# Kernel tuning notes

Measured on AMD Instinct MI355X. Metric: run time of the kernel, lower is better.

Reference implementation:

```python
import jax, jax.numpy as jnp
import numpy as np

E, K, H, F = 16, 4, 1024, 2048
SL, BS = 2048, 2
ALPHA, LIMIT = 1.702, 7.0
CAPACITY_FACTOR = 1.0


def setup_inputs() -> dict:
    key = jax.random.key(0)
    ks = jax.random.split(key, 7)
    x = jax.random.normal(ks[0], (SL, BS, H), jnp.float32)
    router_weight = jax.random.normal(ks[1], (E, H), jnp.float32) * 0.02
    router_bias = jax.random.normal(ks[2], (E,), jnp.float32) * 0.02
    w1 = jax.random.normal(ks[3], (E, H, 2 * F), jnp.float32) * 0.02
    w2 = jax.random.normal(ks[4], (E, F, H), jnp.float32) * 0.02
    w1_bias = jax.random.normal(ks[5], (E, 2 * F), jnp.float32) * 0.02
    w2_bias = jax.random.normal(ks[6], (E, H), jnp.float32) * 0.02
    return {"x": x, "router_weight": router_weight, "router_bias": router_bias,
            "w1": w1, "w2": w2, "w1_bias": w1_bias, "w2_bias": w2_bias}


def reference(x, router_weight, router_bias, w1, w2, w1_bias, w2_bias):
    sl, bs, h = x.shape
    T = sl * bs                      # total tokens
    N = T * K                        # total routed copies
    C = int(CAPACITY_FACTOR * K * T / E)  # static expert capacity
    xf = x.reshape(T, h)

    # --- route_tokens ---
    logits = xf @ router_weight.T + router_bias            # [T, E]
    expert_weights, expert_indices = jax.lax.top_k(logits, K)  # [T, K]
    expert_weights = jax.nn.softmax(expert_weights, axis=-1)
    router_scores = jnp.zeros_like(logits).at[
        jnp.arange(T)[:, None], expert_indices].set(expert_weights).T  # [E, T]

    # --- indices_and_bins: stable sort by expert + histogram ---
    te = expert_indices.reshape(-1)                        # [N] expert id per copy
    ew = expert_weights.reshape(-1)                        # [N] weight per copy
    order = jnp.argsort(te)                                # stable sort -> permutation
    tokens_per_expert = jnp.zeros((E,), jnp.int32).at[te].add(1)
    starts = jnp.cumsum(tokens_per_expert) - tokens_per_expert  # exclusive cumsum

    # --- binned_gather: [E, C, H], overflow tokens dropped, underfull slots zero ---
    j = jnp.arange(C)
    pos = starts[:, None] + j[None, :]                     # [E, C] position in sorted order
    valid = j[None, :] < tokens_per_expert[:, None]        # [E, C]
    flat_idx = order[jnp.clip(pos, 0, N - 1)]              # [E, C] index into flattened copies
    tok = flat_idx // K                                    # [E, C] source token row
    xb = jnp.where(valid[..., None], xf[tok], 0.0)         # [E, C, H]

    # --- mlp_forward: interleaved GLU ---
    gate_up = jnp.einsum('ech,ehf->ecf', xb, w1) + w1_bias[:, None, :]  # [E, C, 2F]
    gate = jnp.minimum(gate_up[..., ::2], LIMIT)
    up = jnp.clip(gate_up[..., 1::2], -LIMIT, LIMIT)
    glu = gate * jax.nn.sigmoid(gate * ALPHA)
    y = jnp.einsum('ecf,efh->ech', (up + 1.0) * glu, w2) + w2_bias[:, None, :]  # [E, C, H]

    # --- binned_scatter: weighted combine back to token rows ---
    w = jnp.where(valid, ew[flat_idx], 0.0)                # [E, C]
    out = jnp.zeros((T, h), x.dtype).at[tok.reshape(-1)].add(
        (w[..., None] * y).reshape(-1, h))
    return out.reshape(sl, bs, h), expert_weights, router_scores
```

## Files before the change

kernel.cpp:

```cpp
#include <hip/hip_runtime.h>
#include <hip/hip_bf16.h>

#define T_TOK 4096
#define E_EXP 16
#define TOPK 4
#define HDIM 1024
#define FDIM 2048
#define CAP 1024
#define NCOPY (T_TOK*TOPK)

typedef __bf16 bf16x8 __attribute__((ext_vector_type(8)));
typedef __bf16 bf16x4 __attribute__((ext_vector_type(4)));
typedef float  f32x4  __attribute__((ext_vector_type(4)));

__global__ __launch_bounds__(64) void router_kernel(
    const float* __restrict__ x, const float* __restrict__ rw, const float* __restrict__ rb,
    float* __restrict__ ew_out, float* __restrict__ rs_out, int* __restrict__ te_out)
{
    int t = blockIdx.x;
    int lane = threadIdx.x;
    const float* xr = x + (size_t)t * HDIM;
    float xv[16];
#pragma unroll
    for (int i = 0; i < 16; ++i) xv[i] = xr[i * 64 + lane];
    float lg[E_EXP];
#pragma unroll
    for (int e = 0; e < E_EXP; ++e) {
        const float* wrow = rw + (size_t)e * HDIM;
        float s = 0.f;
#pragma unroll
        for (int i = 0; i < 16; ++i) s += xv[i] * wrow[i * 64 + lane];
#pragma unroll
        for (int off = 32; off > 0; off >>= 1) s += __shfl_xor(s, off, 64);
        lg[e] = s + rb[e];
    }
    int mask = 0; float vals[4]; int idxs[4];
#pragma unroll
    for (int k = 0; k < 4; ++k) {
        float m = -3.4e38f; int a = 0;
#pragma unroll
        for (int e = 0; e < E_EXP; ++e) {
            bool take = (((mask >> e) & 1) == 0) && (lg[e] > m);
            m = take ? lg[e] : m;
            a = take ? e : a;
        }
        vals[k] = m; idxs[k] = a; mask |= (1 << a);
    }
    float wk[4]; float ssum = 0.f;
#pragma unroll
    for (int k = 0; k < 4; ++k) { wk[k] = __expf(vals[k] - vals[0]); ssum += wk[k]; }
    float inv = 1.f / ssum;
#pragma unroll
    for (int k = 0; k < 4; ++k) wk[k] *= inv;
    if (lane < 4) {
        float wv = 0.f; int iv = 0;
#pragma unroll
        for (int k = 0; k < 4; ++k) if (lane == k) { wv = wk[k]; iv = idxs[k]; }
        ew_out[t * 4 + lane] = wv;
        te_out[t * 4 + lane] = iv;
    }
    if (lane < E_EXP) {
        float v = 0.f;
#pragma unroll
        for (int k = 0; k < 4; ++k) v = (idxs[k] == lane) ? wk[k] : v;
        rs_out[(size_t)lane * T_TOK + t] = v;
    }
}

__global__ __launch_bounds__(256) void binning_kernel(
    const int* __restrict__ te, const float* __restrict__ ew,
    int* __restrict__ slot_tok, float* __restrict__ slot_w)
{
    __shared__ int cnt[256][17];
    int tid = threadIdx.x;
#pragma unroll
    for (int e = 0; e < E_EXP; ++e) cnt[tid][e] = 0;
    __syncthreads();
    int base = tid * 64;
    for (int i = 0; i < 64; ++i) cnt[tid][te[base + i]]++;
    __syncthreads();
    if (tid < E_EXP) {
        int run = 0;
        for (int t2 = 0; t2 < 256; ++t2) { int v = cnt[t2][tid]; cnt[t2][tid] = run; run += v; }
    }
    __syncthreads();
    for (int s = tid; s < E_EXP * CAP; s += 256) { slot_tok[s] = -1; slot_w[s] = 0.f; }
    __syncthreads();
    for (int i = 0; i < 64; ++i) {
        int idx = base + i;
        int e = te[idx];
        int r = cnt[tid][e]; cnt[tid][e] = r + 1;
        if (r < CAP) { slot_tok[e * CAP + r] = idx >> 2; slot_w[e * CAP + r] = ew[idx]; }
    }
}

__global__ __launch_bounds__(256) void gather_kernel(
    const float* __restrict__ x, const int* __restrict__ slot_tok, __bf16* __restrict__ xg)
{
    int s = blockIdx.x, tid = threadIdx.x;
    int tok = slot_tok[s];
    bf16x4 o;
    if (tok >= 0) {
        float4 v = *(const float4*)(x + (size_t)tok * HDIM + tid * 4);
        o[0] = (__bf16)v.x; o[1] = (__bf16)v.y; o[2] = (__bf16)v.z; o[3] = (__bf16)v.w;
    } else {
        o[0] = (__bf16)0.f; o[1] = (__bf16)0.f; o[2] = (__bf16)0.f; o[3] = (__bf16)0.f;
    }
    *(bf16x4*)(xg + (size_t)s * HDIM + tid * 4) = o;
}

__global__ __launch_bounds__(256) void transpose_cvt_kernel(
    const float* __restrict__ in, __bf16* __restrict__ out, int R, int Cc, int tilesR, int tilesC)
{
    __shared__ __bf16 tile[64][68];
    int bx = blockIdx.x;
    int tpe = tilesR * tilesC;
    int e = bx / tpe; int rem = bx - e * tpe;
    int tr = rem / tilesC; int tc = rem - tr * tilesC;
    const float* ine = in + (size_t)e * R * Cc;
    __bf16* oute = out + (size_t)e * R * Cc;
    int r0 = tr * 64, c0 = tc * 64;
    int tid = threadIdx.x;
    int rr = tid >> 4, c4 = (tid & 15) << 2;
#pragma unroll
    for (int it = 0; it < 4; ++it) {
        int r = rr + it * 16;
        float4 v = *(const float4*)(ine + (size_t)(r0 + r) * Cc + c0 + c4);
        tile[r][c4 + 0] = (__bf16)v.x; tile[r][c4 + 1] = (__bf16)v.y;
        tile[r][c4 + 2] = (__bf16)v.z; tile[r][c4 + 3] = (__bf16)v.w;
    }
    __syncthreads();
#pragma unroll
    for (int it = 0; it < 4; ++it) {
        int c = rr + it * 16;
        bf16x4 o;
        o[0] = tile[c4 + 0][c]; o[1] = tile[c4 + 1][c];
        o[2] = tile[c4 + 2][c]; o[3] = tile[c4 + 3][c];
        *(bf16x4*)(oute + (size_t)(c0 + c) * R + r0 + c4) = o;
    }
}

__global__ __launch_bounds__(256) void zero_kernel(float4* p)
{
    p[(size_t)blockIdx.x * 256 + threadIdx.x] = make_float4(0.f, 0.f, 0.f, 0.f);
}

template <int EPI>
__global__ __launch_bounds__(256) void gemm_kernel(
    const __bf16* __restrict__ A, const __bf16* __restrict__ Bt, const float* __restrict__ bias,
    __bf16* __restrict__ actout, float* __restrict__ out,
    const int* __restrict__ slot_tok, const float* __restrict__ slot_w,
    int Kd, int tilesM, int tilesN, int N)
{
    __shared__ __bf16 at[128 * 32];
    __shared__ __bf16 bts[128 * 32];
    int bx = blockIdx.x;
    int tpe = tilesM * tilesN;
    int e = bx / tpe; int rem = bx - e * tpe;
    int bm = rem / tilesN; int bn = rem - bm * tilesN;
    const __bf16* Ab = A + (size_t)e * 1024 * Kd + (size_t)(bm * 128) * Kd;
    const __bf16* Bb = Bt + (size_t)e * N * Kd + (size_t)(bn * 128) * Kd;
    int tid = threadIdx.x;
    int c0 = tid, c1 = tid + 256;
    int ar0 = c0 >> 2, ak0 = (c0 & 3) << 3;
    int ar1 = c1 >> 2, ak1 = (c1 & 3) << 3;

    uint4 ra0 = *(const uint4*)(Ab + (size_t)ar0 * Kd + ak0);
    uint4 ra1 = *(const uint4*)(Ab + (size_t)ar1 * Kd + ak1);
    uint4 rb0 = *(const uint4*)(Bb + (size_t)ar0 * Kd + ak0);
    uint4 rb1 = *(const uint4*)(Bb + (size_t)ar1 * Kd + ak1);

    f32x4 zero4 = {0.f, 0.f, 0.f, 0.f};
    f32x4 acc[4][4];
#pragma unroll
    for (int mi = 0; mi < 4; ++mi)
#pragma unroll
        for (int ni = 0; ni < 4; ++ni) acc[mi][ni] = zero4;

    int w = tid >> 6, l = tid & 63;
    int q = l >> 4, ln = l & 15;
    int wr = (w >> 1) << 6, wc = (w & 1) << 6;

    for (int k0 = 0; k0 < Kd; k0 += 32) {
        *(uint4*)(at + c0 * 8) = ra0;
        *(uint4*)(at + c1 * 8) = ra1;
        *(uint4*)(bts + c0 * 8) = rb0;
        *(uint4*)(bts + c1 * 8) = rb1;
        int kn = k0 + 32;
        if (kn < Kd) {
            ra0 = *(const uint4*)(Ab + (size_t)ar0 * Kd + kn + ak0);
            ra1 = *(const uint4*)(Ab + (size_t)ar1 * Kd + kn + ak1);
            rb0 = *(const uint4*)(Bb + (size_t)ar0 * Kd + kn + ak0);
            rb1 = *(const uint4*)(Bb + (size_t)ar1 * Kd + kn + ak1);
        }
        __syncthreads();
        bf16x8 af[4], bfr[4];
#pragma unroll
        for (int mi = 0; mi < 4; ++mi)
            af[mi] = *(const bf16x8*)(at + (wr + mi * 16 + ln) * 32 + q * 8);
#pragma unroll
        for (int ni = 0; ni < 4; ++ni)
            bfr[ni] = *(const bf16x8*)(bts + (wc + ni * 16 + ln) * 32 + q * 8);
#pragma unroll
        for (int mi = 0; mi < 4; ++mi)
#pragma unroll
            for (int ni = 0; ni < 4; ++ni)
                acc[mi][ni] = __builtin_amdgcn_mfma_f32_16x16x32_bf16(af[mi], bfr[ni], acc[mi][ni], 0, 0, 0);
        __syncthreads();
    }

    float bv[4];
#pragma unroll
    for (int ni = 0; ni < 4; ++ni) bv[ni] = bias[(size_t)e * N + bn * 128 + wc + ni * 16 + ln];

    if constexpr (EPI == 0) {
        __bf16* act_e = actout + (size_t)e * 1024 * FDIM;
#pragma unroll
        for (int mi = 0; mi < 4; ++mi)
#pragma unroll
            for (int ni = 0; ni < 4; ++ni)
#pragma unroll
                for (int r = 0; r < 4; ++r) {
                    int m = bm * 128 + wr + mi * 16 + q * 4 + r;
                    int n = bn * 128 + wc + ni * 16 + ln;
                    float v = acc[mi][ni][r] + bv[ni];
                    float o = __shfl_xor(v, 1, 64);
                    float gate = (ln & 1) ? o : v;
                    float up   = (ln & 1) ? v : o;
                    gate = fminf(gate, 7.f);
                    up = fminf(fmaxf(up, -7.f), 7.f);
                    float glu = gate / (1.f + __expf(-1.702f * gate));
                    float a = (up + 1.f) * glu;
                    if ((ln & 1) == 0) act_e[(size_t)m * FDIM + (n >> 1)] = (__bf16)a;
                }
    } else {
#pragma unroll
        for (int mi = 0; mi < 4; ++mi)
#pragma unroll
            for (int r = 0; r < 4; ++r) {
                int m = bm * 128 + wr + mi * 16 + q * 4 + r;
                int tok = slot_tok[e * CAP + m];
                float wgt = slot_w[e * CAP + m];
                if (tok >= 0) {
#pragma unroll
                    for (int ni = 0; ni < 4; ++ni) {
                        int n = bn * 128 + wc + ni * 16 + ln;
                        float v = (acc[mi][ni][r] + bv[ni]) * wgt;
                        unsafeAtomicAdd(out + (size_t)tok * HDIM + n, v);
                    }
                }
            }
    }
}

extern "C" void kernel_launch(void* const* d_in, const int* in_sizes, int n_in,
                              void* d_out, int out_size, void* d_ws, size_t ws_size,
                              hipStream_t stream)
{
    const float* x  = (const float*)d_in[0];
    const float* rw = (const float*)d_in[1];
    const float* rb = (const float*)d_in[2];
    const float* w1 = (const float*)d_in[3];
    const float* w2 = (const float*)d_in[4];
    const float* b1 = (const float*)d_in[5];
    const float* b2 = (const float*)d_in[6];
    float* out_main = (float*)d_out;
    float* ew_out = out_main + (size_t)T_TOK * HDIM;
    float* rs_out = ew_out + (size_t)T_TOK * TOPK;

    char* ws = (char*)d_ws;
    size_t off = 0;
    auto alloc = [&](size_t bytes) { void* p = ws + off; off += (bytes + 255) & ~(size_t)255; return p; };
    __bf16* w1t = (__bf16*)alloc((size_t)E_EXP * 2 * FDIM * HDIM * 2);
    __bf16* w2t = (__bf16*)alloc((size_t)E_EXP * HDIM * FDIM * 2);
    __bf16* xg  = (__bf16*)alloc((size_t)E_EXP * CAP * HDIM * 2);
    __bf16* act = (__bf16*)alloc((size_t)E_EXP * CAP * FDIM * 2);
    int*   te       = (int*)alloc((size_t)NCOPY * 4);
    int*   slot_tok = (int*)alloc((size_t)E_EXP * CAP * 4);
    float* slot_w   = (float*)alloc((size_t)E_EXP * CAP * 4);

    zero_kernel<<<(T_TOK * HDIM) / 1024, 256, 0, stream>>>((float4*)out_main);
    router_kernel<<<T_TOK, 64, 0, stream>>>(x, rw, rb, ew_out, rs_out, te);
    binning_kernel<<<1, 256, 0, stream>>>(te, ew_out, slot_tok, slot_w);
    gather_kernel<<<E_EXP * CAP, 256, 0, stream>>>(x, slot_tok, xg);
    transpose_cvt_kernel<<<E_EXP * (HDIM / 64) * (2 * FDIM / 64), 256, 0, stream>>>(
        w1, w1t, HDIM, 2 * FDIM, HDIM / 64, 2 * FDIM / 64);
    transpose_cvt_kernel<<<E_EXP * (FDIM / 64) * (HDIM / 64), 256, 0, stream>>>(
        w2, w2t, FDIM, HDIM, FDIM / 64, HDIM / 64);
    gemm_kernel<0><<<E_EXP * 8 * 32, 256, 0, stream>>>(
        xg, w1t, b1, act, nullptr, nullptr, nullptr, HDIM, 8, 32, 2 * FDIM);
    gemm_kernel<1><<<E_EXP * 8 * 8, 256, 0, stream>>>(
        act, w2t, b2, nullptr, out_main, slot_tok, slot_w, FDIM, 8, 8, HDIM);
}
```

Measured before the change: 911.3 us.

## Replace atomic scatter with bf16 expert output plus gather combine; use async LDS loads

The second GEMM no longer scatters weighted results into the output with float atomics. It writes a per-expert bf16 output buffer, which reuses the gather buffer. A new combine kernel then reads each token's up to four slots, through a new slot_of map built during binning, and writes the weighted sum. This removes the output zeroing kernel and the atomic contention. The GEMM main loop now fills LDS with direct global_load_lds transfers instead of a register-staged prefetch. That drops the register staging but also removes the overlap between the next tile's load and the current tile's MFMA work. Storing the expert output in bf16 adds rounding before the combine.

```diff
diff --git a/kernel.cpp b/kernel.cpp
--- a/kernel.cpp
+++ b/kernel.cpp
@@ -13,6 +13,14 @@
 typedef __bf16 bf16x4 __attribute__((ext_vector_type(4)));
 typedef float  f32x4  __attribute__((ext_vector_type(4)));
 
+__device__ __forceinline__ void async16(const __bf16* g, __bf16* l)
+{
+    __builtin_amdgcn_global_load_lds(
+        (const __attribute__((address_space(1))) unsigned int*)g,
+        (__attribute__((address_space(3))) unsigned int*)l,
+        16, 0, 0);
+}
+
 __global__ __launch_bounds__(64) void router_kernel(
     const float* __restrict__ x, const float* __restrict__ rw, const float* __restrict__ rb,
     float* __restrict__ ew_out, float* __restrict__ rs_out, int* __restrict__ te_out)
@@ -68,8 +76,8 @@
 }
 
 __global__ __launch_bounds__(256) void binning_kernel(
-    const int* __restrict__ te, const float* __restrict__ ew,
-    int* __restrict__ slot_tok, float* __restrict__ slot_w)
+    const int* __restrict__ te,
+    int* __restrict__ slot_tok, int* __restrict__ slot_of)
 {
     __shared__ int cnt[256][17];
     int tid = threadIdx.x;
@@ -84,13 +92,14 @@
         for (int t2 = 0; t2 < 256; ++t2) { int v = cnt[t2][tid]; cnt[t2][tid] = run; run += v; }
     }
     __syncthreads();
-    for (int s = tid; s < E_EXP * CAP; s += 256) { slot_tok[s] = -1; slot_w[s] = 0.f; }
+    for (int s = tid; s < E_EXP * CAP; s += 256) slot_tok[s] = -1;
     __syncthreads();
     for (int i = 0; i < 64; ++i) {
         int idx = base + i;
         int e = te[idx];
         int r = cnt[tid][e]; cnt[tid][e] = r + 1;
-        if (r < CAP) { slot_tok[e * CAP + r] = idx >> 2; slot_w[e * CAP + r] = ew[idx]; }
+        if (r < CAP) { slot_tok[e * CAP + r] = idx >> 2; slot_of[idx] = e * CAP + r; }
+        else slot_of[idx] = -1;
     }
 }
 
@@ -140,17 +149,10 @@
     }
 }
 
-__global__ __launch_bounds__(256) void zero_kernel(float4* p)
-{
-    p[(size_t)blockIdx.x * 256 + threadIdx.x] = make_float4(0.f, 0.f, 0.f, 0.f);
-}
-
 template <int EPI>
 __global__ __launch_bounds__(256) void gemm_kernel(
     const __bf16* __restrict__ A, const __bf16* __restrict__ Bt, const float* __restrict__ bias,
-    __bf16* __restrict__ actout, float* __restrict__ out,
-    const int* __restrict__ slot_tok, const float* __restrict__ slot_w,
-    int Kd, int tilesM, int tilesN, int N)
+    __bf16* __restrict__ outp, int Kd, int tilesM, int tilesN, int N)
 {
     __shared__ __bf16 at[128 * 32];
     __shared__ __bf16 bts[128 * 32];
@@ -165,10 +167,14 @@
     int ar0 = c0 >> 2, ak0 = (c0 & 3) << 3;
     int ar1 = c1 >> 2, ak1 = (c1 & 3) << 3;
 
-    uint4 ra0 = *(const uint4*)(Ab + (size_t)ar0 * Kd + ak0);
-    uint4 ra1 = *(const uint4*)(Ab + (size_t)ar1 * Kd + ak1);
-    uint4 rb0 = *(const uint4*)(Bb + (size_t)ar0 * Kd + ak0);
-    uint4 rb1 = *(const uint4*)(Bb + (size_t)ar1 * Kd + ak1);
+    const __bf16* gA0 = Ab + (size_t)ar0 * Kd + ak0;
+    const __bf16* gA1 = Ab + (size_t)ar1 * Kd + ak1;
+    const __bf16* gB0 = Bb + (size_t)ar0 * Kd + ak0;
+    const __bf16* gB1 = Bb + (size_t)ar1 * Kd + ak1;
+    __bf16* lA0 = at + c0 * 8;
+    __bf16* lA1 = at + c1 * 8;
+    __bf16* lB0 = bts + c0 * 8;
+    __bf16* lB1 = bts + c1 * 8;
 
     f32x4 zero4 = {0.f, 0.f, 0.f, 0.f};
     f32x4 acc[4][4];
@@ -182,17 +188,10 @@
     int wr = (w >> 1) << 6, wc = (w & 1) << 6;
 
     for (int k0 = 0; k0 < Kd; k0 += 32) {
-        *(uint4*)(at + c0 * 8) = ra0;
-        *(uint4*)(at + c1 * 8) = ra1;
-        *(uint4*)(bts + c0 * 8) = rb0;
-        *(uint4*)(bts + c1 * 8) = rb1;
-        int kn = k0 + 32;
-        if (kn < Kd) {
-            ra0 = *(const uint4*)(Ab + (size_t)ar0 * Kd + kn + ak0);
-            ra1 = *(const uint4*)(Ab + (size_t)ar1 * Kd + kn + ak1);
-            rb0 = *(const uint4*)(Bb + (size_t)ar0 * Kd + kn + ak0);
-            rb1 = *(const uint4*)(Bb + (size_t)ar1 * Kd + kn + ak1);
-        }
+        async16(gA0 + k0, lA0);
+        async16(gA1 + k0, lA1);
+        async16(gB0 + k0, lB0);
+        async16(gB1 + k0, lB1);
         __syncthreads();
         bf16x8 af[4], bfr[4];
 #pragma unroll
@@ -214,7 +213,7 @@
     for (int ni = 0; ni < 4; ++ni) bv[ni] = bias[(size_t)e * N + bn * 128 + wc + ni * 16 + ln];
 
     if constexpr (EPI == 0) {
-        __bf16* act_e = actout + (size_t)e * 1024 * FDIM;
+        __bf16* act_e = outp + (size_t)e * 1024 * FDIM;
 #pragma unroll
         for (int mi = 0; mi < 4; ++mi)
 #pragma unroll
@@ -234,23 +233,38 @@
                     if ((ln & 1) == 0) act_e[(size_t)m * FDIM + (n >> 1)] = (__bf16)a;
                 }
     } else {
+        __bf16* y_e = outp + (size_t)e * 1024 * HDIM;
 #pragma unroll
         for (int mi = 0; mi < 4; ++mi)
 #pragma unroll
-            for (int r = 0; r < 4; ++r) {
-                int m = bm * 128 + wr + mi * 16 + q * 4 + r;
-                int tok = slot_tok[e * CAP + m];
-                float wgt = slot_w[e * CAP + m];
-                if (tok >= 0) {
-#pragma unroll
-                    for (int ni = 0; ni < 4; ++ni) {
-                        int n = bn * 128 + wc + ni * 16 + ln;
-                        float v = (acc[mi][ni][r] + bv[ni]) * wgt;
-                        unsafeAtomicAdd(out + (size_t)tok * HDIM + n, v);
-                    }
+            for (int ni = 0; ni < 4; ++ni)
+#pragma unroll
+                for (int r = 0; r < 4; ++r) {
+                    int m = bm * 128 + wr + mi * 16 + q * 4 + r;
+                    int n = bn * 128 + wc + ni * 16 + ln;
+                    y_e[(size_t)m * HDIM + n] = (__bf16)(acc[mi][ni][r] + bv[ni]);
                 }
-            }
-    }
+    }
+}
+
+__global__ __launch_bounds__(256) void combine_kernel(
+    const __bf16* __restrict__ y, const int* __restrict__ slot_of,
+    const float* __restrict__ ew, float* __restrict__ out)
+{
+    int t = blockIdx.x, tid = threadIdx.x;
+    float a0 = 0.f, a1 = 0.f, a2 = 0.f, a3 = 0.f;
+#pragma unroll
+    for (int k = 0; k < 4; ++k) {
+        int s = slot_of[t * 4 + k];
+        if (s >= 0) {
+            float wk = ew[t * 4 + k];
+            bf16x4 v = *(const bf16x4*)(y + (size_t)s * HDIM + tid * 4);
+            a0 += wk * (float)v[0]; a1 += wk * (float)v[1];
+            a2 += wk * (float)v[2]; a3 += wk * (float)v[3];
+        }
+    }
+    float4 o = make_float4(a0, a1, a2, a3);
+    *(float4*)(out + (size_t)t * HDIM + tid * 4) = o;
 }
 
 extern "C" void kernel_launch(void* const* d_in, const int* in_sizes, int n_in,
@@ -277,18 +291,19 @@
     __bf16* act = (__bf16*)alloc((size_t)E_EXP * CAP * FDIM * 2);
     int*   te       = (int*)alloc((size_t)NCOPY * 4);
     int*   slot_tok = (int*)alloc((size_t)E_EXP * CAP * 4);
-    float* slot_w   = (float*)alloc((size_t)E_EXP * CAP * 4);
-
-    zero_kernel<<<(T_TOK * HDIM) / 1024, 256, 0, stream>>>((float4*)out_main);
+    int*   slot_of  = (int*)alloc((size_t)NCOPY * 4);
+    __bf16* y = xg;
+
     router_kernel<<<T_TOK, 64, 0, stream>>>(x, rw, rb, ew_out, rs_out, te);
-    binning_kernel<<<1, 256, 0, stream>>>(te, ew_out, slot_tok, slot_w);
+    binning_kernel<<<1, 256, 0, stream>>>(te, slot_tok, slot_of);
     gather_kernel<<<E_EXP * CAP, 256, 0, stream>>>(x, slot_tok, xg);
     transpose_cvt_kernel<<<E_EXP * (HDIM / 64) * (2 * FDIM / 64), 256, 0, stream>>>(
         w1, w1t, HDIM, 2 * FDIM, HDIM / 64, 2 * FDIM / 64);
     transpose_cvt_kernel<<<E_EXP * (FDIM / 64) * (HDIM / 64), 256, 0, stream>>>(
         w2, w2t, FDIM, HDIM, FDIM / 64, HDIM / 64);
     gemm_kernel<0><<<E_EXP * 8 * 32, 256, 0, stream>>>(
-        xg, w1t, b1, act, nullptr, nullptr, nullptr, HDIM, 8, 32, 2 * FDIM);
+        xg, w1t, b1, act, HDIM, 8, 32, 2 * FDIM);
     gemm_kernel<1><<<E_EXP * 8 * 8, 256, 0, stream>>>(
-        act, w2t, b2, nullptr, out_main, slot_tok, slot_w, FDIM, 8, 8, HDIM);
-}
+        act, w2t, b2, y, FDIM, 8, 8, HDIM);
+    combine_kernel<<<T_TOK, 256, 0, stream>>>(y, slot_of, ew_out, out_main);
+}
```

New measurement: 936.9 us. 1.03x slower.
